# Optimization experiments

Measured on AMD Instinct MI355X. Metric: run time of the kernel, lower is better.

The kernel has to match this reference:

```python
import jax, jax.numpy as jnp
import numpy as np

B, H, W, C = 2, 128, 128, 128
NS = 8                      # attn_num_splits
WH, WW = H // NS, W // NS   # window size 16x16
SH, SW = WH // 2, WW // 2   # shift sizes
HID = 2 * C * 4             # ffn hidden (in_channels = 2*d_model, expansion 4)
EPS = 1e-5


def _make_swin_mask():
    # Standard shifted-window attention mask: -100 between different regions.
    img = np.zeros((H, W), np.int32)
    cnt = 0
    for hs in (slice(0, -WH), slice(-WH, -SH), slice(-SH, None)):
        for ws in (slice(0, -WW), slice(-WW, -SW), slice(-SW, None)):
            img[hs, ws] = cnt
            cnt += 1
    ids = img.reshape(NS, WH, NS, WW).transpose(0, 2, 1, 3).reshape(NS * NS, WH * WW)
    mask = np.where(ids[:, None, :] != ids[:, :, None], -100.0, 0.0).astype(np.float32)
    return jnp.asarray(mask)  # (64, 256, 256)


def _layernorm(x, g, b):
    m = jnp.mean(x, axis=-1, keepdims=True)
    v = jnp.mean(jnp.square(x - m), axis=-1, keepdims=True)
    return (x - m) * jax.lax.rsqrt(v + EPS) * g + b


def setup_inputs() -> dict:
    key = jax.random.key(0)
    ks = jax.random.split(key, 8)
    s = 1.0 / np.sqrt(C)
    return {
        "source": jax.random.normal(ks[0], (B, H * W, C), jnp.float32),
        "target": jax.random.normal(ks[1], (B, H * W, C), jnp.float32),
        "Wq": jax.random.normal(ks[2], (C, C), jnp.float32) * s,
        "Wk": jax.random.normal(ks[3], (C, C), jnp.float32) * s,
        "Wv": jax.random.normal(ks[4], (C, C), jnp.float32) * s,
        "Wm": jax.random.normal(ks[5], (C, C), jnp.float32) * s,
        "g1": jnp.ones((C,), jnp.float32),
        "b1": jnp.zeros((C,), jnp.float32),
        "W1": jax.random.normal(ks[6], (2 * C, HID), jnp.float32) * (1.0 / np.sqrt(2 * C)),
        "W2": jax.random.normal(ks[7], (HID, C), jnp.float32) * (1.0 / np.sqrt(HID)),
        "g2": jnp.ones((C,), jnp.float32),
        "b2": jnp.zeros((C,), jnp.float32),
        "shifted_window_attn_mask": _make_swin_mask(),
        "height": H,
        "width": W,
        "attn_num_splits": NS,
    }


def reference(source, target, Wq, Wk, Wv, Wm, g1, b1, W1, W2, g2, b2,
              shifted_window_attn_mask, height, width, attn_num_splits):
    b, L, c = source.shape
    h, w, ns = height, width, attn_num_splits
    wh, ww = h // ns, w // ns
    sh, sw = wh // 2, ww // 2

    q = source @ Wq
    k = target @ Wk
    v = target @ Wv

    def to_windows(x):
        # (b, h*w, c) -> shifted -> (b, nWin, wh*ww, c)
        x = x.reshape(b, h, w, c)
        x = jnp.roll(x, (-sh, -sw), axis=(1, 2))
        x = x.reshape(b, ns, wh, ns, ww, c).transpose(0, 1, 3, 2, 4, 5)
        return x.reshape(b, ns * ns, wh * ww, c)

    qw, kw, vw = to_windows(q), to_windows(k), to_windows(v)
    scores = jnp.einsum('bnlc,bnmc->bnlm', qw, kw) / (c ** 0.5)
    scores = scores + shifted_window_attn_mask[None]  # broadcast over batch
    attn = jax.nn.softmax(scores, axis=-1)
    out = jnp.einsum('bnlm,bnmc->bnlc', attn, vw)

    # merge windows back and undo the shift
    out = out.reshape(b, ns, ns, wh, ww, c).transpose(0, 1, 3, 2, 4, 5).reshape(b, h, w, c)
    out = jnp.roll(out, (sh, sw), axis=(1, 2)).reshape(b, h * w, c)

    message = _layernorm(out @ Wm, g1, b1)
    ffn_in = jnp.concatenate([source, message], axis=-1)
    message = jax.nn.gelu(ffn_in @ W1, approximate=False) @ W2
    message = _layernorm(message, g2, b2)
    return source + message
```

## Files before the change

### kernel.cpp

```cpp
#include <hip/hip_runtime.h>
#include <math.h>
#include <stdint.h>


typedef unsigned short u16;
typedef __attribute__((ext_vector_type(8))) short bf16x8;
typedef __attribute__((ext_vector_type(4))) float f32x4;
typedef __attribute__((ext_vector_type(16))) float f32x16;
typedef __attribute__((ext_vector_type(4))) short u16x4;

__device__ __forceinline__ u16 f2b(float f) {
    unsigned int i = __float_as_uint(f);
    unsigned int r = (i + 0x7fffu + ((i >> 16) & 1u)) >> 16;
    return (u16)r;
}

__device__ __forceinline__ float gelu_e(float x) {
    float y = fabsf(x) * 0.70710678118f;
    float u = fmaf(y, fmaf(y, fmaf(y, fmaf(y, 0.078108f, 0.000972f),
                                   0.230389f), 0.278393f), 1.0f);
    u = u * u; u = u * u;
    float r = __builtin_amdgcn_rcpf(u);
    return fmaxf(x, 0.f) - 0.5f * fabsf(x) * r;
}

__device__ __forceinline__ void cp16(const void* g, void* l) {
    auto* gp = reinterpret_cast<const __attribute__((address_space(1))) unsigned int*>(
        reinterpret_cast<uintptr_t>(g));
    auto* lp = reinterpret_cast<__attribute__((address_space(3))) unsigned int*>(
        reinterpret_cast<uintptr_t>(l));
    __builtin_amdgcn_global_load_lds(gp, lp, 16, 0, 0);
}

__device__ __forceinline__ int win_map(int gm) {
    int b = gm >> 14, rr = gm & 16383;
    int win = rr >> 8, t = rr & 255;
    int wi = win >> 3, wj = win & 7, i = t >> 4, j = t & 15;
    int h = (wi * 16 + i + 8) & 127;
    int w = (wj * 16 + j + 8) & 127;
    return (b << 14) + h * 128 + w;
}

__global__ __launch_bounds__(256, 2)
void gemm_qkv(const u16* __restrict__ srcb, const u16* __restrict__ tgtb,
              const u16* __restrict__ Bt, u16* __restrict__ qw,
              u16* __restrict__ kw, u16* __restrict__ vwt)
{
    __shared__ __align__(16) u16 SMEM[32768];
    u16* As = SMEM;
    u16* Bs = SMEM + 16384;
    u16* Ts = SMEM;

    const int tid = threadIdx.x;
    const int w = tid >> 6, lane = tid & 63;
    const int lm = lane & 15, q = lane >> 4;
    const int wm = w >> 1, wn = w & 1;
    const int m0 = blockIdx.x * 128;
    const int y = blockIdx.y;
    const u16* Ab = (y == 0) ? srcb : tgtb;

#pragma unroll
    for (int s = 0; s < 4; ++s)
#pragma unroll
        for (int i = 0; i < 2; ++i) {
            int row = w * 32 + i * 16 + (lane >> 2);
            int kc = s * 32 + (lane & 3) * 8;
            cp16(Ab + (size_t)win_map(m0 + row) * 128 + kc,
                 (void*)(As + (s * 128 + w * 32 + i * 16) * 32));
            cp16(Bt + (size_t)(y * 128 + row) * 128 + kc,
                 (void*)(Bs + (s * 128 + w * 32 + i * 16) * 32));
        }
    __syncthreads();

    f32x4 acc[4][4] = {};
#pragma unroll
    for (int s = 0; s < 4; ++s) {
        bf16x8 af[4], bfr[4];
#pragma unroll
        for (int t = 0; t < 4; ++t)
            af[t] = *(const bf16x8*)(As + (s * 128 + wm * 64 + t * 16 + lm) * 32 + q * 8);
#pragma unroll
        for (int t = 0; t < 4; ++t)
            bfr[t] = *(const bf16x8*)(Bs + (s * 128 + wn * 64 + t * 16 + lm) * 32 + q * 8);
#pragma unroll
        for (int mt = 0; mt < 4; ++mt)
#pragma unroll
            for (int nt = 0; nt < 4; ++nt)
                acc[mt][nt] = __builtin_amdgcn_mfma_f32_16x16x32_bf16(
                    af[mt], bfr[nt], acc[mt][nt], 0, 0, 0);
    }

    __syncthreads();
#pragma unroll
    for (int mt = 0; mt < 4; ++mt)
#pragma unroll
        for (int nt = 0; nt < 4; ++nt)
#pragma unroll
            for (int r = 0; r < 4; ++r) {
                int rowl = wm * 64 + mt * 16 + q * 4 + r;
                int col = wn * 64 + nt * 16 + lm;
                int idx = (y == 2) ? col * 136 + rowl : rowl * 136 + col;
                Ts[idx] = f2b(acc[mt][nt][r]);
            }
    __syncthreads();
    const int c8 = (tid & 15) * 8;
#pragma unroll
    for (int i = 0; i < 8; ++i) {
        int rr = i * 16 + (tid >> 4);
        bf16x8 t = *(const bf16x8*)(Ts + rr * 136 + c8);
        if (y == 2) {
            int wix = m0 >> 8, tok0 = m0 & 255;
            *(bf16x8*)(vwt + (size_t)wix * 32768 + (size_t)rr * 256 + tok0 + c8) = t;
        } else {
            u16* Cv = (y == 0) ? qw : kw;
            *(bf16x8*)(Cv + (size_t)(m0 + rr) * 128 + c8) = t;
        }
    }
}

__global__ __launch_bounds__(256, 2)
void gemm_ffn1(const u16* __restrict__ A0, const u16* __restrict__ A1,
               const u16* __restrict__ Bt, u16* __restrict__ C)
{
    __shared__ __align__(16) u16 SMEM[32768];
    u16* As = SMEM;
    u16* Bs = SMEM + 16384;

    const int tid = threadIdx.x;
    const int w = tid >> 6, lane = tid & 63;
    const int l32 = lane & 31, lh = lane >> 5;
    const int wm = w >> 1, wn = w & 1;
    const int m0 = blockIdx.x * 128, n0 = blockIdx.y * 128;

    f32x16 acc[2][2] = {};
#pragma unroll
    for (int kt2 = 0; kt2 < 2; ++kt2) {
        __syncthreads();
        const u16* Ab = kt2 ? A1 : A0;
#pragma unroll
        for (int s = 0; s < 4; ++s)
#pragma unroll
            for (int i = 0; i < 2; ++i) {
                int row = w * 32 + i * 16 + (lane >> 2);
                int kc = s * 32 + (lane & 3) * 8;
                cp16(Ab + (size_t)(m0 + row) * 128 + kc,
                     (void*)(As + (s * 128 + w * 32 + i * 16) * 32));
                cp16(Bt + (size_t)(n0 + row) * 256 + kt2 * 128 + kc,
                     (void*)(Bs + (s * 128 + w * 32 + i * 16) * 32));
            }
        __syncthreads();
#pragma unroll
        for (int s = 0; s < 4; ++s)
#pragma unroll
            for (int kc = 0; kc < 2; ++kc) {
                bf16x8 af[2], bfr[2];
#pragma unroll
                for (int mt = 0; mt < 2; ++mt)
                    af[mt] = *(const bf16x8*)(As + (s * 128 + wm * 64 + mt * 32 + l32) * 32
                                              + kc * 16 + lh * 8);
#pragma unroll
                for (int nt = 0; nt < 2; ++nt)
                    bfr[nt] = *(const bf16x8*)(Bs + (s * 128 + wn * 64 + nt * 32 + l32) * 32
                                               + kc * 16 + lh * 8);
#pragma unroll
                for (int mt = 0; mt < 2; ++mt)
#pragma unroll
                    for (int nt = 0; nt < 2; ++nt)
                        acc[mt][nt] = __builtin_amdgcn_mfma_f32_32x32x16_bf16(
                            af[mt], bfr[nt], acc[mt][nt], 0, 0, 0);
            }
    }

#pragma unroll
    for (int mt = 0; mt < 2; ++mt)
#pragma unroll
        for (int nt = 0; nt < 2; ++nt) {
            int col = n0 + wn * 64 + nt * 32 + l32;
            int rbase = m0 + wm * 64 + mt * 32 + 4 * lh;
#pragma unroll
            for (int r = 0; r < 16; ++r) {
                int row = rbase + (r & 3) + 8 * (r >> 2);
                C[(size_t)row * 1024 + col] = f2b(gelu_e(acc[mt][nt][r]));
            }
        }
}

__global__ __launch_bounds__(256, 2)
void attn_msg(const u16* __restrict__ qw, const u16* __restrict__ kw,
              const u16* __restrict__ vt, const u16* __restrict__ wmt,
              const float* __restrict__ g, const float* __restrict__ bb,
              u16* __restrict__ msgb)
{
    __shared__ __align__(16) u16 Ps[64 * 264];
    __shared__ __align__(16) u16 B32[16384];

    const int tid = threadIdx.x, w = tid >> 6, lane = tid & 63;
    const int lm = lane & 15, q = lane >> 4;
    const int l4r = lane >> 2, l4c = (lane & 3) * 8;
    const int bid = blockIdx.x;
    const int qc = bid & 3, win = (bid >> 2) & 63, b = bid >> 8;
    const int wi = win >> 3, wj = win & 7;
    const int q0 = qc * 64;
    const size_t wbase = (size_t)(b * 64 + win);
    const u16* kwb = kw + wbase * 256 * 128;
    const u16* qwb = qw + wbase * 256 * 128;
    const u16* vtb = vt + wbase * 128 * 256;

    u16* Qs = Ps;
#pragma unroll
    for (int i = 0; i < 4; ++i)
        cp16(qwb + (size_t)(q0 + w * 16 + l4r) * 128 + i * 32 + l4c,
             (void*)(Qs + (i * 64 + w * 16) * 32));
#pragma unroll
    for (int s = 0; s < 4; ++s)
#pragma unroll
        for (int i = 0; i < 2; ++i) {
            int tok = w * 32 + i * 16 + l4r;
            cp16(kwb + (size_t)tok * 128 + s * 32 + l4c,
                 (void*)(B32 + (s * 128 + w * 32 + i * 16) * 32));
        }
    __syncthreads();

    bf16x8 af[4];
#pragma unroll
    for (int kt = 0; kt < 4; ++kt)
        af[kt] = *(const bf16x8*)(Qs + (kt * 64 + w * 16 + lm) * 32 + q * 8);

    f32x4 s[16];
#pragma unroll
    for (int nt = 0; nt < 16; ++nt) { f32x4 z = {0.f, 0.f, 0.f, 0.f}; s[nt] = z; }
#pragma unroll
    for (int kt = 0; kt < 4; ++kt)
#pragma unroll
        for (int nt = 0; nt < 8; ++nt) {
            bf16x8 bf = *(const bf16x8*)(B32 + (kt * 128 + nt * 16 + lm) * 32 + q * 8);
            s[nt] = __builtin_amdgcn_mfma_f32_16x16x32_bf16(af[kt], bf, s[nt], 0, 0, 0);
        }
    __syncthreads();
#pragma unroll
    for (int ss = 0; ss < 4; ++ss)
#pragma unroll
        for (int i = 0; i < 2; ++i) {
            int tok = 128 + w * 32 + i * 16 + l4r;
            cp16(kwb + (size_t)tok * 128 + ss * 32 + l4c,
                 (void*)(B32 + (ss * 128 + w * 32 + i * 16) * 32));
        }
    __syncthreads();
#pragma unroll
    for (int kt = 0; kt < 4; ++kt)
#pragma unroll
        for (int nt = 8; nt < 16; ++nt) {
            bf16x8 bf = *(const bf16x8*)(B32 + (kt * 128 + (nt - 8) * 16 + lm) * 32 + q * 8);
            s[nt] = __builtin_amdgcn_mfma_f32_16x16x32_bf16(af[kt], bf, s[nt], 0, 0, 0);
        }
    __syncthreads();

#pragma unroll
    for (int tt = 0; tt < 4; ++tt)
#pragma unroll
        for (int i = 0; i < 2; ++i) {
            int ch = w * 32 + i * 16 + l4r;
            cp16(vtb + (size_t)ch * 256 + tt * 32 + l4c,
                 (void*)(B32 + (tt * 128 + w * 32 + i * 16) * 32));
        }

    int idk[16];
#pragma unroll
    for (int nt = 0; nt < 16; ++nt) {
        int rh = (wi == 7) ? ((nt >= 8) ? 2 : 1) : 0;
        int rw = (wj == 7) ? ((lm >= 8) ? 2 : 1) : 0;
        idk[nt] = rh * 3 + rw;
    }
    const float scale = 0.08838834764831845f;
#pragma unroll
    for (int r = 0; r < 4; ++r) {
        int tq = q0 + w * 16 + q * 4 + r;
        int iq = tq >> 4, jq = tq & 15;
        int rhq = (wi == 7) ? ((iq >= 8) ? 2 : 1) : 0;
        int rwq = (wj == 7) ? ((jq >= 8) ? 2 : 1) : 0;
        int idq = rhq * 3 + rwq;
        float sv[16];
        float mx = -1e30f;
#pragma unroll
        for (int nt = 0; nt < 16; ++nt) {
            float x = s[nt][r] * scale + ((idq != idk[nt]) ? -100.f : 0.f);
            sv[nt] = x; mx = fmaxf(mx, x);
        }
        mx = fmaxf(mx, __shfl_xor(mx, 1));
        mx = fmaxf(mx, __shfl_xor(mx, 2));
        mx = fmaxf(mx, __shfl_xor(mx, 4));
        mx = fmaxf(mx, __shfl_xor(mx, 8));
        float sum = 0.f;
#pragma unroll
        for (int nt = 0; nt < 16; ++nt) { float e = __expf(sv[nt] - mx); sv[nt] = e; sum += e; }
        sum += __shfl_xor(sum, 1);
        sum += __shfl_xor(sum, 2);
        sum += __shfl_xor(sum, 4);
        sum += __shfl_xor(sum, 8);
        float inv = 1.0f / sum;
#pragma unroll
        for (int nt = 0; nt < 16; ++nt)
            Ps[(w * 16 + q * 4 + r) * 264 + nt * 16 + lm] = f2b(sv[nt] * inv);
    }
    __syncthreads();

    f32x4 o[8];
#pragma unroll
    for (int nt = 0; nt < 8; ++nt) { f32x4 z = {0.f, 0.f, 0.f, 0.f}; o[nt] = z; }
#pragma unroll
    for (int tt = 0; tt < 4; ++tt) {
        bf16x8 pf = *(const bf16x8*)(Ps + (w * 16 + lm) * 264 + tt * 32 + q * 8);
#pragma unroll
        for (int nt = 0; nt < 8; ++nt) {
            bf16x8 vf = *(const bf16x8*)(B32 + (tt * 128 + nt * 16 + lm) * 32 + q * 8);
            o[nt] = __builtin_amdgcn_mfma_f32_16x16x32_bf16(pf, vf, o[nt], 0, 0, 0);
        }
    }
    __syncthreads();
#pragma unroll
    for (int tt = 0; tt < 4; ++tt)
#pragma unroll
        for (int i = 0; i < 2; ++i) {
            int ch = w * 32 + i * 16 + l4r;
            cp16(vtb + (size_t)ch * 256 + 128 + tt * 32 + l4c,
                 (void*)(B32 + (tt * 128 + w * 32 + i * 16) * 32));
        }
    __syncthreads();
#pragma unroll
    for (int tt = 4; tt < 8; ++tt) {
        bf16x8 pf = *(const bf16x8*)(Ps + (w * 16 + lm) * 264 + tt * 32 + q * 8);
#pragma unroll
        for (int nt = 0; nt < 8; ++nt) {
            bf16x8 vf = *(const bf16x8*)(B32 + ((tt - 4) * 128 + nt * 16 + lm) * 32 + q * 8);
            o[nt] = __builtin_amdgcn_mfma_f32_16x16x32_bf16(pf, vf, o[nt], 0, 0, 0);
        }
    }
    __syncthreads();

#pragma unroll
    for (int ss = 0; ss < 4; ++ss)
#pragma unroll
        for (int i = 0; i < 2; ++i) {
            int n = w * 32 + i * 16 + l4r;
            cp16(wmt + (size_t)n * 128 + ss * 32 + l4c,
                 (void*)(B32 + (ss * 128 + w * 32 + i * 16) * 32));
        }
    u16* Ot = Ps;
#pragma unroll
    for (int r = 0; r < 4; ++r) {
        int rl = w * 16 + q * 4 + r;
#pragma unroll
        for (int nt = 0; nt < 8; ++nt)
            Ot[rl * 136 + nt * 16 + lm] = f2b(o[nt][r]);
    }
    __syncthreads();

    f32x4 macc[8];
#pragma unroll
    for (int n2 = 0; n2 < 8; ++n2) { f32x4 z = {0.f, 0.f, 0.f, 0.f}; macc[n2] = z; }
#pragma unroll
    for (int kt = 0; kt < 4; ++kt) {
        bf16x8 paf = *(const bf16x8*)(Ot + (w * 16 + lm) * 136 + kt * 32 + q * 8);
#pragma unroll
        for (int n2 = 0; n2 < 8; ++n2) {
            bf16x8 wf = *(const bf16x8*)(B32 + (kt * 128 + n2 * 16 + lm) * 32 + q * 8);
            macc[n2] = __builtin_amdgcn_mfma_f32_16x16x32_bf16(paf, wf, macc[n2], 0, 0, 0);
        }
    }

    float gv[8], bv[8];
#pragma unroll
    for (int n2 = 0; n2 < 8; ++n2) {
        int col = n2 * 16 + lm;
        gv[n2] = g[col]; bv[n2] = bb[col];
    }
#pragma unroll
    for (int r = 0; r < 4; ++r) {
        float s1 = 0.f, s2 = 0.f;
#pragma unroll
        for (int n2 = 0; n2 < 8; ++n2) {
            float v = macc[n2][r];
            s1 += v; s2 += v * v;
        }
        s1 += __shfl_xor(s1, 1); s2 += __shfl_xor(s2, 1);
        s1 += __shfl_xor(s1, 2); s2 += __shfl_xor(s2, 2);
        s1 += __shfl_xor(s1, 4); s2 += __shfl_xor(s2, 4);
        s1 += __shfl_xor(s1, 8); s2 += __shfl_xor(s2, 8);
        float mean = s1 * (1.f / 128.f);
        float var = fmaxf(s2 * (1.f / 128.f) - mean * mean, 0.f);
        float rs = rsqrtf(var + 1e-5f);
        int t = q0 + w * 16 + q * 4 + r;
        int ii = t >> 4, jj = t & 15;
        int h = (wi * 16 + ii + 8) & 127;
        int w2 = (wj * 16 + jj + 8) & 127;
        size_t orow = ((size_t)b * 16384 + h * 128 + w2) * 128;
#pragma unroll
        for (int n2 = 0; n2 < 8; ++n2)
            msgb[orow + n2 * 16 + lm] = f2b((macc[n2][r] - mean) * rs * gv[n2] + bv[n2]);
    }
}

__global__ __launch_bounds__(256, 3)
void gemm_ffn2(const u16* __restrict__ A, const u16* __restrict__ Bt,
               const float* __restrict__ g, const float* __restrict__ bb,
               const float* __restrict__ resid, float* __restrict__ outv)
{
    __shared__ __align__(16) u16 SMEM[25088];
    u16* As = SMEM;
    u16* Bs = SMEM + 8192;
    float* stats = (float*)(SMEM + 24576);

    const int tid = threadIdx.x;
    const int w = tid >> 6, lane = tid & 63;
    const int lm = lane & 15, q = lane >> 4;
    const int wm = w >> 1, wn = w & 1;
    const int m0 = blockIdx.x * 64;
    const int K = 1024;

    f32x4 acc[2][4] = {};
#pragma unroll
    for (int kt2 = 0; kt2 < 8; ++kt2) {
        __syncthreads();
#pragma unroll
        for (int s = 0; s < 4; ++s) {
            int kc = kt2 * 128 + s * 32 + (lane & 3) * 8;
            int arow = w * 16 + (lane >> 2);
            cp16(A + (size_t)(m0 + arow) * K + kc,
                 (void*)(As + (s * 64 + w * 16) * 32));
#pragma unroll
            for (int i = 0; i < 2; ++i) {
                int brow = w * 32 + i * 16 + (lane >> 2);
                cp16(Bt + (size_t)brow * K + kc,
                     (void*)(Bs + (s * 128 + w * 32 + i * 16) * 32));
            }
        }
        __syncthreads();
#pragma unroll
        for (int s = 0; s < 4; ++s) {
            bf16x8 af[2], bfr[4];
#pragma unroll
            for (int t = 0; t < 2; ++t)
                af[t] = *(const bf16x8*)(As + (s * 64 + wm * 32 + t * 16 + lm) * 32 + q * 8);
#pragma unroll
            for (int t = 0; t < 4; ++t)
                bfr[t] = *(const bf16x8*)(Bs + (s * 128 + wn * 64 + t * 16 + lm) * 32 + q * 8);
#pragma unroll
            for (int mt = 0; mt < 2; ++mt)
#pragma unroll
                for (int nt = 0; nt < 4; ++nt)
                    acc[mt][nt] = __builtin_amdgcn_mfma_f32_16x16x32_bf16(
                        af[mt], bfr[nt], acc[mt][nt], 0, 0, 0);
        }
    }

#pragma unroll
    for (int mt = 0; mt < 2; ++mt)
#pragma unroll
        for (int r = 0; r < 4; ++r) {
            float s1 = 0.f, s2 = 0.f;
#pragma unroll
            for (int nt = 0; nt < 4; ++nt) {
                float v = acc[mt][nt][r];
                s1 += v; s2 += v * v;
            }
            s1 += __shfl_xor(s1, 1); s2 += __shfl_xor(s2, 1);
            s1 += __shfl_xor(s1, 2); s2 += __shfl_xor(s2, 2);
            s1 += __shfl_xor(s1, 4); s2 += __shfl_xor(s2, 4);
            s1 += __shfl_xor(s1, 8); s2 += __shfl_xor(s2, 8);
            if (lm == 0) {
                int row = wm * 32 + mt * 16 + q * 4 + r;
                stats[row * 4 + wn * 2] = s1;
                stats[row * 4 + wn * 2 + 1] = s2;
            }
        }
    __syncthreads();

    float gv[4], bv[4];
#pragma unroll
    for (int nt = 0; nt < 4; ++nt) {
        int col = wn * 64 + nt * 16 + lm;
        gv[nt] = g[col]; bv[nt] = bb[col];
    }
#pragma unroll
    for (int mt = 0; mt < 2; ++mt)
#pragma unroll
        for (int r = 0; r < 4; ++r) {
            int row = wm * 32 + mt * 16 + q * 4 + r;
            f32x4 st = *(const f32x4*)(stats + row * 4);
            float mean = (st[0] + st[2]) * (1.f / 128.f);
            float var = fmaxf((st[1] + st[3]) * (1.f / 128.f) - mean * mean, 0.f);
            float rs = rsqrtf(var + 1e-5f);
#pragma unroll
            for (int nt = 0; nt < 4; ++nt) {
                int col = wn * 64 + nt * 16 + lm;
                size_t gi = (size_t)(m0 + row) * 128 + col;
                outv[gi] = (acc[mt][nt][r] - mean) * rs * gv[nt] + bv[nt] + resid[gi];
            }
        }
}

__global__ void prep_all(const float* __restrict__ Wq, const float* __restrict__ Wk,
                         const float* __restrict__ Wv, const float* __restrict__ Wm,
                         const float* __restrict__ W1, const float* __restrict__ W2,
                         const float* __restrict__ src, const float* __restrict__ tgt,
                         u16* __restrict__ ws, u16* __restrict__ srcb,
                         u16* __restrict__ tgtb)
{
    int bx = blockIdx.x;
    if (bx < 1792) {
        int idx = bx * 256 + threadIdx.x;
        if (idx < 65536) {
            int m = idx >> 14, e = idx & 16383;
            const float* sp = (m == 0) ? Wq : (m == 1) ? Wk : (m == 2) ? Wv : Wm;
            int n = e >> 7, k = e & 127;
            ws[m * 16384 + n * 128 + k] = f2b(sp[k * 128 + n]);
        } else if (idx < 327680) {
            int e = idx - 65536;
            int n = e >> 8, k = e & 255;
            ws[65536 + n * 256 + k] = f2b(W1[k * 1024 + n]);
        } else {
            int e = idx - 327680;
            int n = e >> 10, k = e & 1023;
            ws[327680 + n * 1024 + k] = f2b(W2[k * 128 + n]);
        }
    } else {
        int idx = (bx - 1792) * 256 + threadIdx.x;
        const float* s; u16* d; int i;
        if (idx < 1048576) { s = src; d = srcb; i = idx * 4; }
        else               { s = tgt; d = tgtb; i = (idx - 1048576) * 4; }
        f32x4 v = *(const f32x4*)(s + i);
        u16x4 o; o[0] = f2b(v[0]); o[1] = f2b(v[1]); o[2] = f2b(v[2]); o[3] = f2b(v[3]);
        *(u16x4*)(d + i) = o;
    }
}

#define OFF_WQT  0u
#define OFF_WMT  49152u
#define OFF_W1T  65536u
#define OFF_W2T  327680u
#define OFF_SRCB 458752u
#define OFF_TGTB 4653056u
#define OFF_QW   8847360u
#define OFF_KW   13041664u
#define OFF_VWT  17235968u
#define OFF_MSGB 21430272u
#define OFF_HID  25624576u

extern "C" void kernel_launch(void* const* d_in, const int* in_sizes, int n_in,
                              void* d_out, int out_size, void* d_ws, size_t ws_size,
                              hipStream_t stream)
{
    (void)in_sizes; (void)n_in; (void)out_size; (void)ws_size;
    const float* source = (const float*)d_in[0];
    const float* target = (const float*)d_in[1];
    const float* Wq = (const float*)d_in[2];
    const float* Wk = (const float*)d_in[3];
    const float* Wv = (const float*)d_in[4];
    const float* Wm = (const float*)d_in[5];
    const float* g1 = (const float*)d_in[6];
    const float* b1 = (const float*)d_in[7];
    const float* W1 = (const float*)d_in[8];
    const float* W2 = (const float*)d_in[9];
    const float* g2 = (const float*)d_in[10];
    const float* b2 = (const float*)d_in[11];
    u16* ws = (u16*)d_ws;
    float* out = (float*)d_out;

    prep_all<<<9984, 256, 0, stream>>>(Wq, Wk, Wv, Wm, W1, W2, source, target,
                                       ws, ws + OFF_SRCB, ws + OFF_TGTB);
    gemm_qkv<<<dim3(256, 3), 256, 0, stream>>>(
        ws + OFF_SRCB, ws + OFF_TGTB, ws + OFF_WQT,
        ws + OFF_QW, ws + OFF_KW, ws + OFF_VWT);
    attn_msg<<<512, 256, 0, stream>>>(
        ws + OFF_QW, ws + OFF_KW, ws + OFF_VWT, ws + OFF_WMT, g1, b1,
        ws + OFF_MSGB);
    gemm_ffn1<<<dim3(256, 8), 256, 0, stream>>>(
        ws + OFF_SRCB, ws + OFF_MSGB, ws + OFF_W1T, ws + OFF_HID);
    gemm_ffn2<<<512, 256, 0, stream>>>(
        ws + OFF_HID, ws + OFF_W2T, g2, b2, source, out);
}
```

Before: 207.8 us.

## Retile FFN GEMMs with padded LDS and tiled weight transpose

Both FFN GEMM kernels now stage smaller K=64 tiles through registers into padded LDS rows (stride 68), replacing the direct global-to-LDS copies. The aim is to cut LDS use so occupancy can rise to 4 blocks per CU. FFN2 switches from 16x16 to 32x32 MFMA tiles with a new LayerNorm reduction. The weight-prep kernel now transposes through a shared-memory tile so global reads are coalesced. Register staging gives up the async LDS load path, and the 8-byte split LDS accesses may add instruction overhead.

```diff
diff --git a/kernel.cpp b/kernel.cpp
--- a/kernel.cpp
+++ b/kernel.cpp
@@ -5,6 +5,7 @@
 
 typedef unsigned short u16;
 typedef __attribute__((ext_vector_type(8))) short bf16x8;
+typedef __attribute__((ext_vector_type(4))) short s16x4;
 typedef __attribute__((ext_vector_type(4))) float f32x4;
 typedef __attribute__((ext_vector_type(16))) float f32x16;
 typedef __attribute__((ext_vector_type(4))) short u16x4;
@@ -30,6 +31,22 @@
     auto* lp = reinterpret_cast<__attribute__((address_space(3))) unsigned int*>(
         reinterpret_cast<uintptr_t>(l));
     __builtin_amdgcn_global_load_lds(gp, lp, 16, 0, 0);
+}
+
+__device__ __forceinline__ void st_lds8(u16* p, bf16x8 v) {
+    s16x4 lo, hi;
+    lo[0] = v[0]; lo[1] = v[1]; lo[2] = v[2]; lo[3] = v[3];
+    hi[0] = v[4]; hi[1] = v[5]; hi[2] = v[6]; hi[3] = v[7];
+    *(s16x4*)p = lo;
+    *(s16x4*)(p + 4) = hi;
+}
+__device__ __forceinline__ bf16x8 ld_lds8(const u16* p) {
+    s16x4 lo = *(const s16x4*)p;
+    s16x4 hi = *(const s16x4*)(p + 4);
+    bf16x8 r;
+    r[0] = lo[0]; r[1] = lo[1]; r[2] = lo[2]; r[3] = lo[3];
+    r[4] = hi[0]; r[5] = hi[1]; r[6] = hi[2]; r[7] = hi[3];
+    return r;
 }
 
 __device__ __forceinline__ int win_map(int gm) {
@@ -118,57 +135,54 @@
     }
 }
 
-__global__ __launch_bounds__(256, 2)
+__global__ __launch_bounds__(256, 4)
 void gemm_ffn1(const u16* __restrict__ A0, const u16* __restrict__ A1,
                const u16* __restrict__ Bt, u16* __restrict__ C)
 {
-    __shared__ __align__(16) u16 SMEM[32768];
-    u16* As = SMEM;
-    u16* Bs = SMEM + 16384;
+    __shared__ __align__(16) u16 As[128 * 68];
+    __shared__ __align__(16) u16 Bs[128 * 68];
 
     const int tid = threadIdx.x;
-    const int w = tid >> 6, lane = tid & 63;
+    const int lane = tid & 63, w = tid >> 6;
     const int l32 = lane & 31, lh = lane >> 5;
     const int wm = w >> 1, wn = w & 1;
     const int m0 = blockIdx.x * 128, n0 = blockIdx.y * 128;
 
     f32x16 acc[2][2] = {};
 #pragma unroll
-    for (int kt2 = 0; kt2 < 2; ++kt2) {
+    for (int kt = 0; kt < 4; ++kt) {
+        const u16* Ab = (kt < 2) ? A0 : A1;
+        const int ka = (kt & 1) * 64;
         __syncthreads();
-        const u16* Ab = kt2 ? A1 : A0;
-#pragma unroll
-        for (int s = 0; s < 4; ++s)
-#pragma unroll
-            for (int i = 0; i < 2; ++i) {
-                int row = w * 32 + i * 16 + (lane >> 2);
-                int kc = s * 32 + (lane & 3) * 8;
-                cp16(Ab + (size_t)(m0 + row) * 128 + kc,
-                     (void*)(As + (s * 128 + w * 32 + i * 16) * 32));
-                cp16(Bt + (size_t)(n0 + row) * 256 + kt2 * 128 + kc,
-                     (void*)(Bs + (s * 128 + w * 32 + i * 16) * 32));
-            }
+#pragma unroll
+        for (int i = 0; i < 4; ++i) {
+            int id = i * 256 + tid, row = id >> 3, c = id & 7;
+            bf16x8 v = *(const bf16x8*)(Ab + (size_t)(m0 + row) * 128 + ka + c * 8);
+            st_lds8(As + row * 68 + c * 8, v);
+        }
+#pragma unroll
+        for (int i = 0; i < 4; ++i) {
+            int id = i * 256 + tid, row = id >> 3, c = id & 7;
+            bf16x8 v = *(const bf16x8*)(Bt + (size_t)(n0 + row) * 256 + kt * 64 + c * 8);
+            st_lds8(Bs + row * 68 + c * 8, v);
+        }
         __syncthreads();
 #pragma unroll
-        for (int s = 0; s < 4; ++s)
-#pragma unroll
-            for (int kc = 0; kc < 2; ++kc) {
-                bf16x8 af[2], bfr[2];
-#pragma unroll
-                for (int mt = 0; mt < 2; ++mt)
-                    af[mt] = *(const bf16x8*)(As + (s * 128 + wm * 64 + mt * 32 + l32) * 32
-                                              + kc * 16 + lh * 8);
+        for (int kc = 0; kc < 4; ++kc) {
+            bf16x8 af[2], bfr[2];
+#pragma unroll
+            for (int mt = 0; mt < 2; ++mt)
+                af[mt] = ld_lds8(As + (wm * 64 + mt * 32 + l32) * 68 + kc * 16 + lh * 8);
+#pragma unroll
+            for (int nt = 0; nt < 2; ++nt)
+                bfr[nt] = ld_lds8(Bs + (wn * 64 + nt * 32 + l32) * 68 + kc * 16 + lh * 8);
+#pragma unroll
+            for (int mt = 0; mt < 2; ++mt)
 #pragma unroll
                 for (int nt = 0; nt < 2; ++nt)
-                    bfr[nt] = *(const bf16x8*)(Bs + (s * 128 + wn * 64 + nt * 32 + l32) * 32
-                                               + kc * 16 + lh * 8);
-#pragma unroll
-                for (int mt = 0; mt < 2; ++mt)
-#pragma unroll
-                    for (int nt = 0; nt < 2; ++nt)
-                        acc[mt][nt] = __builtin_amdgcn_mfma_f32_32x32x16_bf16(
-                            af[mt], bfr[nt], acc[mt][nt], 0, 0, 0);
-            }
+                    acc[mt][nt] = __builtin_amdgcn_mfma_f32_32x32x16_bf16(
+                        af[mt], bfr[nt], acc[mt][nt], 0, 0, 0);
+        }
     }
 
 #pragma unroll
@@ -183,6 +197,88 @@
                 C[(size_t)row * 1024 + col] = f2b(gelu_e(acc[mt][nt][r]));
             }
         }
+}
+
+__global__ __launch_bounds__(256, 4)
+void gemm_ffn2(const u16* __restrict__ A, const u16* __restrict__ Bt,
+               const float* __restrict__ g, const float* __restrict__ bb,
+               const float* __restrict__ resid, float* __restrict__ outv)
+{
+    __shared__ __align__(16) u16 As[64 * 68];
+    __shared__ __align__(16) u16 Bs[128 * 68];
+    __shared__ float stats[64][2][2];
+
+    const int tid = threadIdx.x;
+    const int lane = tid & 63, w = tid >> 6;
+    const int l32 = lane & 31, lh = lane >> 5;
+    const int wm = w >> 1, wn = w & 1;
+    const int m0 = blockIdx.x * 64;
+
+    f32x16 acc[2] = {};
+#pragma unroll
+    for (int kt = 0; kt < 16; ++kt) {
+        __syncthreads();
+#pragma unroll
+        for (int i = 0; i < 2; ++i) {
+            int id = i * 256 + tid, row = id >> 3, c = id & 7;
+            bf16x8 v = *(const bf16x8*)(A + (size_t)(m0 + row) * 1024 + kt * 64 + c * 8);
+            st_lds8(As + row * 68 + c * 8, v);
+        }
+#pragma unroll
+        for (int i = 0; i < 4; ++i) {
+            int id = i * 256 + tid, row = id >> 3, c = id & 7;
+            bf16x8 v = *(const bf16x8*)(Bt + (size_t)row * 1024 + kt * 64 + c * 8);
+            st_lds8(Bs + row * 68 + c * 8, v);
+        }
+        __syncthreads();
+#pragma unroll
+        for (int kc = 0; kc < 4; ++kc) {
+            bf16x8 af = ld_lds8(As + (wm * 32 + l32) * 68 + kc * 16 + lh * 8);
+            bf16x8 bf0 = ld_lds8(Bs + (wn * 64 + l32) * 68 + kc * 16 + lh * 8);
+            bf16x8 bf1 = ld_lds8(Bs + (wn * 64 + 32 + l32) * 68 + kc * 16 + lh * 8);
+            acc[0] = __builtin_amdgcn_mfma_f32_32x32x16_bf16(af, bf0, acc[0], 0, 0, 0);
+            acc[1] = __builtin_amdgcn_mfma_f32_32x32x16_bf16(af, bf1, acc[1], 0, 0, 0);
+        }
+    }
+
+#pragma unroll
+    for (int r = 0; r < 16; ++r) {
+        float v0 = acc[0][r], v1 = acc[1][r];
+        float s1 = v0 + v1, s2 = v0 * v0 + v1 * v1;
+        s1 += __shfl_xor(s1, 1);  s2 += __shfl_xor(s2, 1);
+        s1 += __shfl_xor(s1, 2);  s2 += __shfl_xor(s2, 2);
+        s1 += __shfl_xor(s1, 4);  s2 += __shfl_xor(s2, 4);
+        s1 += __shfl_xor(s1, 8);  s2 += __shfl_xor(s2, 8);
+        s1 += __shfl_xor(s1, 16); s2 += __shfl_xor(s2, 16);
+        if (l32 == 0) {
+            int row = wm * 32 + (r & 3) + 8 * (r >> 2) + 4 * lh;
+            stats[row][wn][0] = s1;
+            stats[row][wn][1] = s2;
+        }
+    }
+    __syncthreads();
+
+    float gv[2], bv[2];
+#pragma unroll
+    for (int nt = 0; nt < 2; ++nt) {
+        int col = wn * 64 + nt * 32 + l32;
+        gv[nt] = g[col]; bv[nt] = bb[col];
+    }
+#pragma unroll
+    for (int r = 0; r < 16; ++r) {
+        int row = wm * 32 + (r & 3) + 8 * (r >> 2) + 4 * lh;
+        float s1 = stats[row][0][0] + stats[row][1][0];
+        float s2 = stats[row][0][1] + stats[row][1][1];
+        float mean = s1 * (1.f / 128.f);
+        float var = fmaxf(s2 * (1.f / 128.f) - mean * mean, 0.f);
+        float rs = rsqrtf(var + 1e-5f);
+#pragma unroll
+        for (int nt = 0; nt < 2; ++nt) {
+            int col = wn * 64 + nt * 32 + l32;
+            size_t gi = (size_t)(m0 + row) * 128 + col;
+            outv[gi] = (acc[nt][r] - mean) * rs * gv[nt] + bv[nt] + resid[gi];
+        }
+    }
 }
 
 __global__ __launch_bounds__(256, 2)
@@ -400,105 +496,6 @@
     }
 }
 
-__global__ __launch_bounds__(256, 3)
-void gemm_ffn2(const u16* __restrict__ A, const u16* __restrict__ Bt,
-               const float* __restrict__ g, const float* __restrict__ bb,
-               const float* __restrict__ resid, float* __restrict__ outv)
-{
-    __shared__ __align__(16) u16 SMEM[25088];
-    u16* As = SMEM;
-    u16* Bs = SMEM + 8192;
-    float* stats = (float*)(SMEM + 24576);
-
-    const int tid = threadIdx.x;
-    const int w = tid >> 6, lane = tid & 63;
-    const int lm = lane & 15, q = lane >> 4;
-    const int wm = w >> 1, wn = w & 1;
-    const int m0 = blockIdx.x * 64;
-    const int K = 1024;
-
-    f32x4 acc[2][4] = {};
-#pragma unroll
-    for (int kt2 = 0; kt2 < 8; ++kt2) {
-        __syncthreads();
-#pragma unroll
-        for (int s = 0; s < 4; ++s) {
-            int kc = kt2 * 128 + s * 32 + (lane & 3) * 8;
-            int arow = w * 16 + (lane >> 2);
-            cp16(A + (size_t)(m0 + arow) * K + kc,
-                 (void*)(As + (s * 64 + w * 16) * 32));
-#pragma unroll
-            for (int i = 0; i < 2; ++i) {
-                int brow = w * 32 + i * 16 + (lane >> 2);
-                cp16(Bt + (size_t)brow * K + kc,
-                     (void*)(Bs + (s * 128 + w * 32 + i * 16) * 32));
-            }
-        }
-        __syncthreads();
-#pragma unroll
-        for (int s = 0; s < 4; ++s) {
-            bf16x8 af[2], bfr[4];
-#pragma unroll
-            for (int t = 0; t < 2; ++t)
-                af[t] = *(const bf16x8*)(As + (s * 64 + wm * 32 + t * 16 + lm) * 32 + q * 8);
-#pragma unroll
-            for (int t = 0; t < 4; ++t)
-                bfr[t] = *(const bf16x8*)(Bs + (s * 128 + wn * 64 + t * 16 + lm) * 32 + q * 8);
-#pragma unroll
-            for (int mt = 0; mt < 2; ++mt)
-#pragma unroll
-                for (int nt = 0; nt < 4; ++nt)
-                    acc[mt][nt] = __builtin_amdgcn_mfma_f32_16x16x32_bf16(
-                        af[mt], bfr[nt], acc[mt][nt], 0, 0, 0);
-        }
-    }
-
-#pragma unroll
-    for (int mt = 0; mt < 2; ++mt)
-#pragma unroll
-        for (int r = 0; r < 4; ++r) {
-            float s1 = 0.f, s2 = 0.f;
-#pragma unroll
-            for (int nt = 0; nt < 4; ++nt) {
-                float v = acc[mt][nt][r];
-                s1 += v; s2 += v * v;
-            }
-            s1 += __shfl_xor(s1, 1); s2 += __shfl_xor(s2, 1);
-            s1 += __shfl_xor(s1, 2); s2 += __shfl_xor(s2, 2);
-            s1 += __shfl_xor(s1, 4); s2 += __shfl_xor(s2, 4);
-            s1 += __shfl_xor(s1, 8); s2 += __shfl_xor(s2, 8);
-            if (lm == 0) {
-                int row = wm * 32 + mt * 16 + q * 4 + r;
-                stats[row * 4 + wn * 2] = s1;
-                stats[row * 4 + wn * 2 + 1] = s2;
-            }
-        }
-    __syncthreads();
-
-    float gv[4], bv[4];
-#pragma unroll
-    for (int nt = 0; nt < 4; ++nt) {
-        int col = wn * 64 + nt * 16 + lm;
-        gv[nt] = g[col]; bv[nt] = bb[col];
-    }
-#pragma unroll
-    for (int mt = 0; mt < 2; ++mt)
-#pragma unroll
-        for (int r = 0; r < 4; ++r) {
-            int row = wm * 32 + mt * 16 + q * 4 + r;
-            f32x4 st = *(const f32x4*)(stats + row * 4);
-            float mean = (st[0] + st[2]) * (1.f / 128.f);
-            float var = fmaxf((st[1] + st[3]) * (1.f / 128.f) - mean * mean, 0.f);
-            float rs = rsqrtf(var + 1e-5f);
-#pragma unroll
-            for (int nt = 0; nt < 4; ++nt) {
-                int col = wn * 64 + nt * 16 + lm;
-                size_t gi = (size_t)(m0 + row) * 128 + col;
-                outv[gi] = (acc[mt][nt][r] - mean) * rs * gv[nt] + bv[nt] + resid[gi];
-            }
-        }
-}
-
 __global__ void prep_all(const float* __restrict__ Wq, const float* __restrict__ Wk,
                          const float* __restrict__ Wv, const float* __restrict__ Wm,
                          const float* __restrict__ W1, const float* __restrict__ W2,
@@ -506,25 +503,38 @@
                          u16* __restrict__ ws, u16* __restrict__ srcb,
                          u16* __restrict__ tgtb)
 {
+    __shared__ float T[64][65];
     int bx = blockIdx.x;
-    if (bx < 1792) {
-        int idx = bx * 256 + threadIdx.x;
-        if (idx < 65536) {
-            int m = idx >> 14, e = idx & 16383;
-            const float* sp = (m == 0) ? Wq : (m == 1) ? Wk : (m == 2) ? Wv : Wm;
-            int n = e >> 7, k = e & 127;
-            ws[m * 16384 + n * 128 + k] = f2b(sp[k * 128 + n]);
-        } else if (idx < 327680) {
-            int e = idx - 65536;
-            int n = e >> 8, k = e & 255;
-            ws[65536 + n * 256 + k] = f2b(W1[k * 1024 + n]);
+    if (bx < 112) {
+        const float* sp; u16* dst; int R, C, r0, c0;
+        if (bx < 16) {
+            int m = bx >> 2;
+            sp = (m == 0) ? Wq : (m == 1) ? Wk : (m == 2) ? Wv : Wm;
+            dst = ws + m * 16384; R = 128; C = 128;
+            r0 = ((bx >> 1) & 1) * 64; c0 = (bx & 1) * 64;
+        } else if (bx < 80) {
+            int e = bx - 16;
+            sp = W1; dst = ws + 65536; R = 256; C = 1024;
+            r0 = (e >> 4) * 64; c0 = (e & 15) * 64;
         } else {
-            int e = idx - 327680;
-            int n = e >> 10, k = e & 1023;
-            ws[327680 + n * 1024 + k] = f2b(W2[k * 128 + n]);
+            int e = bx - 80;
+            sp = W2; dst = ws + 327680; R = 1024; C = 128;
+            r0 = (e >> 1) * 64; c0 = (e & 1) * 64;
+        }
+        int tc = threadIdx.x & 63, tg = threadIdx.x >> 6;
+#pragma unroll
+        for (int i = 0; i < 16; ++i) {
+            int r = tg * 16 + i;
+            T[r][tc] = sp[(size_t)(r0 + r) * C + c0 + tc];
+        }
+        __syncthreads();
+#pragma unroll
+        for (int j = 0; j < 16; ++j) {
+            int cc = tg * 16 + j;
+            dst[(size_t)(c0 + cc) * R + r0 + tc] = f2b(T[tc][cc]);
         }
     } else {
-        int idx = (bx - 1792) * 256 + threadIdx.x;
+        int idx = (bx - 112) * 256 + threadIdx.x;
         const float* s; u16* d; int i;
         if (idx < 1048576) { s = src; d = srcb; i = idx * 4; }
         else               { s = tgt; d = tgtb; i = (idx - 1048576) * 4; }
@@ -566,8 +576,8 @@
     u16* ws = (u16*)d_ws;
     float* out = (float*)d_out;
 
-    prep_all<<<9984, 256, 0, stream>>>(Wq, Wk, Wv, Wm, W1, W2, source, target,
-                                       ws, ws + OFF_SRCB, ws + OFF_TGTB);
+    prep_all<<<112 + 8192, 256, 0, stream>>>(Wq, Wk, Wv, Wm, W1, W2, source, target,
+                                             ws, ws + OFF_SRCB, ws + OFF_TGTB);
     gemm_qkv<<<dim3(256, 3), 256, 0, stream>>>(
         ws + OFF_SRCB, ws + OFF_TGTB, ws + OFF_WQT,
         ws + OFF_QW, ws + OFF_KW, ws + OFF_VWT);
```

Result: slower. 229.5 us (+10.4%).
